# Kernel optimization log

Hardware: AMD Instinct MI355X
Metric: run time of the kernel (lower is better)

The kernel has to match this reference:

```python
import jax, jax.numpy as jnp
import numpy as np

B, S, HID = 1, 2048, 2048
H, KV, D = 16, 8, 128          # heads, kv heads, head_dim
EPS = 1e-6
THETA_T, THETA_HW = 1000000.0, 10000.0
SCALE = D ** -0.5
NEG = -1e9


def _rms(x, w):
    xf = x.astype(jnp.float32)
    var = jnp.mean(xf * xf, axis=-1, keepdims=True)
    return (w * (xf * jax.lax.rsqrt(var + EPS))).astype(x.dtype)


def _rope_cs(pos, theta, half_dim):
    # Module builds RoPE with head_dim = 2*half_dim then takes every-other freq:
    # exponents arange(0, 2*half_dim, 4) / (2*half_dim)  -> half_dim//2 freqs
    dim2 = 2 * half_dim
    inv_freq = 1.0 / theta ** (jnp.arange(0, dim2, 4, dtype=jnp.float32) / dim2)
    freqs = pos.astype(jnp.float32)[:, None] * inv_freq[None, :]   # [S, half_dim//2]
    emb = jnp.concatenate([freqs, freqs], axis=-1)                 # [S, half_dim]
    return jnp.cos(emb), jnp.sin(emb)


def _rot_half(x):
    d = x.shape[-1] // 2
    return jnp.concatenate([-x[..., d:], x[..., :d]], axis=-1)


def _apply_rope(q, k, cos, sin):
    cos = cos[None, None]  # [1,1,S,dim]
    sin = sin[None, None]
    return q * cos + _rot_half(q) * sin, k * cos + _rot_half(k) * sin


def setup_inputs() -> dict:
    key = jax.random.key(0)
    ks = jax.random.split(key, 10)
    hidden_states = jax.random.normal(ks[0], (B, S, HID), jnp.float32)
    indexes = jax.random.randint(ks[1], (3, S), 0, S)
    causal = jnp.tril(jnp.ones((S, S), bool))
    attention_mask = jnp.where(causal, 0.0, NEG).astype(jnp.float32)[None, None]
    qkv_w = jax.random.normal(ks[2], ((H + 2 * KV) * D, HID), jnp.float32) * 0.02
    qkv_b = jax.random.normal(ks[3], ((H + 2 * KV) * D,), jnp.float32) * 0.02
    o_w = jax.random.normal(ks[4], (HID, H * D), jnp.float32) * 0.02
    o_b = jax.random.normal(ks[5], (HID,), jnp.float32) * 0.02
    q_norm_w = jnp.ones((D // 2,), jnp.float32)
    k_norm_w = jnp.ones((D // 2,), jnp.float32)
    q_norm_hw_w = jnp.ones((D // 2,), jnp.float32)
    k_norm_hw_w = jnp.ones((D // 2,), jnp.float32)
    return dict(hidden_states=hidden_states, indexes=indexes, attention_mask=attention_mask,
                qkv_w=qkv_w, qkv_b=qkv_b, o_w=o_w, o_b=o_b,
                q_norm_w=q_norm_w, k_norm_w=k_norm_w,
                q_norm_hw_w=q_norm_hw_w, k_norm_hw_w=k_norm_hw_w)


def reference(hidden_states, indexes, attention_mask, qkv_w, qkv_b, o_w, o_b,
              q_norm_w, k_norm_w, q_norm_hw_w, k_norm_hw_w):
    b, s, _ = hidden_states.shape
    qkv = hidden_states @ qkv_w.T + qkv_b
    q, k, v = jnp.split(qkv, [H * D, H * D + KV * D], axis=-1)
    q = q.reshape(b, s, H, D)
    k = k.reshape(b, s, KV, D)
    v = v.reshape(b, s, KV, D)

    # split head_dim into time half and hw half
    q_t, q_hw = jnp.split(q, 2, axis=-1)
    k_t, k_hw = jnp.split(k, 2, axis=-1)
    q_t = jnp.swapaxes(_rms(q_t, q_norm_w), 1, 2)       # [B,H,S,D/2]
    k_t = jnp.swapaxes(_rms(k_t, k_norm_w), 1, 2)
    q_hw = jnp.swapaxes(_rms(q_hw, q_norm_hw_w), 1, 2)
    k_hw = jnp.swapaxes(_rms(k_hw, k_norm_hw_w), 1, 2)
    q_h, q_ww = jnp.split(q_hw, 2, axis=-1)             # [B,H,S,D/4]
    k_h, k_ww = jnp.split(k_hw, 2, axis=-1)

    cos_t, sin_t = _rope_cs(indexes[0], THETA_T, D // 2)
    q_t, k_t = _apply_rope(q_t, k_t, cos_t, sin_t)
    cos_h, sin_h = _rope_cs(indexes[1], THETA_HW, D // 4)
    q_h, k_h = _apply_rope(q_h, k_h, cos_h, sin_h)
    cos_w, sin_w = _rope_cs(indexes[2], THETA_HW, D // 4)
    q_ww, k_ww = _apply_rope(q_ww, k_ww, cos_w, sin_w)

    query = jnp.concatenate([q_t, q_h, q_ww], axis=-1)  # [B,H,S,D]
    keyst = jnp.concatenate([k_t, k_h, k_ww], axis=-1)  # [B,KV,S,D]
    value = jnp.swapaxes(v, 1, 2)                       # [B,KV,S,D]

    n_rep = H // KV
    keyst = jnp.repeat(keyst, n_rep, axis=1)
    value = jnp.repeat(value, n_rep, axis=1)

    scores = jnp.einsum('bhsd,bhtd->bhst', query, keyst) * SCALE + attention_mask
    probs = jax.nn.softmax(scores.astype(jnp.float32), axis=-1).astype(query.dtype)
    attn = jnp.einsum('bhst,bhtd->bhsd', probs, value)
    attn = jnp.swapaxes(attn, 1, 2).reshape(b, s, H * D)
    return attn @ o_w.T + o_b
```

## Files before the change

### kernel.cpp

```cpp
#include <hip/hip_runtime.h>

typedef __bf16 bf16;
typedef __bf16 bf16x4 __attribute__((ext_vector_type(4)));
typedef __bf16 bf16x8 __attribute__((ext_vector_type(8)));
typedef float f32x4 __attribute__((ext_vector_type(4)));

#define S_LEN 2048
#define HIDDEN 2048
#define NH 16
#define NKV 8
#define HD 128
#define QKV_N 4096

#define PSLOT 66560

__device__ __forceinline__ void async_load16(const void* g, void* l) {
  __builtin_amdgcn_global_load_lds((const __attribute__((address_space(1))) unsigned int*)g,
                                   (__attribute__((address_space(3))) unsigned int*)l,
                                   16, 0, 0);
}

template <int C>
__device__ __forceinline__ float dpp_f(float x) {
  return __builtin_bit_cast(float, __builtin_amdgcn_mov_dpp(
      __builtin_bit_cast(int, x), C, 0xF, 0xF, true));
}
__device__ __forceinline__ float rowmax16(float x) {
  x = fmaxf(x, dpp_f<0x128>(x));
  x = fmaxf(x, dpp_f<0x124>(x));
  x = fmaxf(x, dpp_f<0x122>(x));
  x = fmaxf(x, dpp_f<0x121>(x));
  return x;
}
__device__ __forceinline__ float rowsum16(float x) {
  x += dpp_f<0x128>(x);
  x += dpp_f<0x124>(x);
  x += dpp_f<0x122>(x);
  x += dpp_f<0x121>(x);
  return x;
}

__global__ __launch_bounds__(256)
void cvt_pair(const float* __restrict__ s1, bf16* __restrict__ d1, int n1,
              const float* __restrict__ s2, bf16* __restrict__ d2, int n2) {
  int i = (blockIdx.x * 256 + threadIdx.x) * 4;
  const float* s;
  bf16* d;
  int j;
  if (i < n1) { s = s1; d = d1; j = i; }
  else        { s = s2; d = d2; j = i - n1; if (j >= n2) return; }
  float4 v = *(const float4*)(s + j);
  bf16x4 o = {(bf16)v.x, (bf16)v.y, (bf16)v.z, (bf16)v.w};
  *(bf16x4*)(d + j) = o;
}

template <int WRITE_BF16>
__global__ __launch_bounds__(256)
void gemm_bt(const bf16* __restrict__ A, const bf16* __restrict__ B,
             const float* __restrict__ bias, void* __restrict__ Cout,
             int M, int N, int K) {
  __shared__ bf16 As[2][128 * 64];
  __shared__ bf16 Bs[2][128 * 64];
  const int tid = threadIdx.x;
  const int w = tid >> 6, lane = tid & 63;
  const int quad = lane >> 4, l15 = lane & 15;
  const int wm = w >> 1, wn = w & 1;
  const int m0 = blockIdx.y * 128, n0 = blockIdx.x * 128;

  f32x4 acc[4][4];
#pragma unroll
  for (int i = 0; i < 4; i++)
#pragma unroll
    for (int j = 0; j < 4; j++) acc[i][j] = (f32x4){0.f, 0.f, 0.f, 0.f};

  const int crow = lane >> 2;
  const int ccol = (lane & 3) * 8;

#pragma unroll
  for (int q = 0; q < 4; q++) {
    int c = w * 4 + q, rb = c >> 1, kh = c & 1;
    async_load16(A + (size_t)(m0 + rb * 16 + crow) * K + kh * 32 + ccol,
                 (char*)As[0] + c * 1024);
    async_load16(B + (size_t)(n0 + rb * 16 + crow) * K + kh * 32 + ccol,
                 (char*)Bs[0] + c * 1024);
  }

  int cur = 0;
  for (int k0 = 0; k0 < K; k0 += 64) {
    __asm__ __volatile__("s_waitcnt vmcnt(0)" ::: "memory");
    __syncthreads();
    if (k0 + 64 < K) {
#pragma unroll
      for (int q = 0; q < 4; q++) {
        int c = w * 4 + q, rb = c >> 1, kh = c & 1;
        async_load16(A + (size_t)(m0 + rb * 16 + crow) * K + k0 + 64 + kh * 32 + ccol,
                     (char*)As[cur ^ 1] + c * 1024);
        async_load16(B + (size_t)(n0 + rb * 16 + crow) * K + k0 + 64 + kh * 32 + ccol,
                     (char*)Bs[cur ^ 1] + c * 1024);
      }
    }
    bf16x8 af[4][2], bfr[4][2];
#pragma unroll
    for (int i = 0; i < 4; i++)
#pragma unroll
      for (int kk = 0; kk < 2; kk++)
        af[i][kk] = *(const bf16x8*)((const char*)As[cur] +
                                     ((wm * 4 + i) * 2 + kk) * 1024 + l15 * 64 + quad * 16);
#pragma unroll
    for (int j = 0; j < 4; j++)
#pragma unroll
      for (int kk = 0; kk < 2; kk++)
        bfr[j][kk] = *(const bf16x8*)((const char*)Bs[cur] +
                                      ((wn * 4 + j) * 2 + kk) * 1024 + l15 * 64 + quad * 16);
#pragma unroll
    for (int kk = 0; kk < 2; kk++)
#pragma unroll
      for (int i = 0; i < 4; i++)
#pragma unroll
        for (int j = 0; j < 4; j++)
          acc[i][j] = __builtin_amdgcn_mfma_f32_16x16x32_bf16(af[i][kk], bfr[j][kk],
                                                              acc[i][j], 0, 0, 0);
    cur ^= 1;
  }

#pragma unroll
  for (int i = 0; i < 4; i++) {
#pragma unroll
    for (int j = 0; j < 4; j++) {
      int col = n0 + wn * 64 + j * 16 + l15;
      float bv = bias[col];
#pragma unroll
      for (int r = 0; r < 4; r++) {
        int row = m0 + wm * 64 + i * 16 + quad * 4 + r;
        float v = acc[i][j][r] + bv;
        if (WRITE_BF16)
          ((bf16*)Cout)[(size_t)row * N + col] = (bf16)v;
        else
          ((float*)Cout)[(size_t)row * N + col] = v;
      }
    }
  }
}

__global__ __launch_bounds__(256)
void gemm_qkv(const bf16* __restrict__ A, const bf16* __restrict__ B,
              const float* __restrict__ bias, const int* __restrict__ idx,
              const float* __restrict__ qnw, const float* __restrict__ knw,
              const float* __restrict__ qnhw, const float* __restrict__ knhw,
              bf16* __restrict__ Qb, bf16* __restrict__ Kb, bf16* __restrict__ VT) {
  const int K = HIDDEN;
  __shared__ __align__(16) char smem[128 * 132 * 4];
  char* Abase = smem;
  char* Bbase = smem + 32768;
  const int tid = threadIdx.x;
  const int w = tid >> 6, lane = tid & 63;
  const int quad = lane >> 4, l15 = lane & 15;
  const int wm = w >> 1, wn = w & 1;
  const int m0 = blockIdx.y * 128, n0 = blockIdx.x * 128;

  f32x4 acc[4][4];
#pragma unroll
  for (int i = 0; i < 4; i++)
#pragma unroll
    for (int j = 0; j < 4; j++) acc[i][j] = (f32x4){0.f, 0.f, 0.f, 0.f};

  const int crow = lane >> 2;
  const int ccol = (lane & 3) * 8;

#pragma unroll
  for (int q = 0; q < 4; q++) {
    int c = w * 4 + q, rb = c >> 1, kh = c & 1;
    async_load16(A + (size_t)(m0 + rb * 16 + crow) * K + kh * 32 + ccol,
                 Abase + c * 1024);
    async_load16(B + (size_t)(n0 + rb * 16 + crow) * K + kh * 32 + ccol,
                 Bbase + c * 1024);
  }

  int cur = 0;
  for (int k0 = 0; k0 < K; k0 += 64) {
    __asm__ __volatile__("s_waitcnt vmcnt(0)" ::: "memory");
    __syncthreads();
    if (k0 + 64 < K) {
#pragma unroll
      for (int q = 0; q < 4; q++) {
        int c = w * 4 + q, rb = c >> 1, kh = c & 1;
        async_load16(A + (size_t)(m0 + rb * 16 + crow) * K + k0 + 64 + kh * 32 + ccol,
                     Abase + (cur ^ 1) * 16384 + c * 1024);
        async_load16(B + (size_t)(n0 + rb * 16 + crow) * K + k0 + 64 + kh * 32 + ccol,
                     Bbase + (cur ^ 1) * 16384 + c * 1024);
      }
    }
    bf16x8 af[4][2], bfr[4][2];
#pragma unroll
    for (int i = 0; i < 4; i++)
#pragma unroll
      for (int kk = 0; kk < 2; kk++)
        af[i][kk] = *(const bf16x8*)(Abase + cur * 16384 +
                                     ((wm * 4 + i) * 2 + kk) * 1024 + l15 * 64 + quad * 16);
#pragma unroll
    for (int j = 0; j < 4; j++)
#pragma unroll
      for (int kk = 0; kk < 2; kk++)
        bfr[j][kk] = *(const bf16x8*)(Bbase + cur * 16384 +
                                      ((wn * 4 + j) * 2 + kk) * 1024 + l15 * 64 + quad * 16);
#pragma unroll
    for (int kk = 0; kk < 2; kk++)
#pragma unroll
      for (int i = 0; i < 4; i++)
#pragma unroll
        for (int j = 0; j < 4; j++)
          acc[i][j] = __builtin_amdgcn_mfma_f32_16x16x32_bf16(af[i][kk], bfr[j][kk],
                                                              acc[i][j], 0, 0, 0);
    cur ^= 1;
  }

  const int nb = blockIdx.x;

  if (nb >= 24) {
    const int kv = nb - 24;
#pragma unroll
    for (int i = 0; i < 4; i++) {
#pragma unroll
      for (int j = 0; j < 4; j++) {
        const int d = wn * 64 + j * 16 + l15;
        const float bv = bias[n0 + d];
        bf16x4 o;
#pragma unroll
        for (int r = 0; r < 4; r++) o[r] = (bf16)(acc[i][j][r] + bv);
        *(bf16x4*)(VT + ((size_t)(kv * HD + d)) * S_LEN +
                   (m0 + wm * 64 + i * 16 + quad * 4)) = o;
      }
    }
    return;
  }

  __syncthreads();
  float* tile = (float*)smem;
#pragma unroll
  for (int i = 0; i < 4; i++) {
#pragma unroll
    for (int j = 0; j < 4; j++) {
      const int col = wn * 64 + j * 16 + l15;
      const float bv = bias[n0 + col];
      const int row = wm * 64 + i * 16 + quad * 4;
#pragma unroll
      for (int r = 0; r < 4; r++)
        tile[(row + r) * 132 + col] = acc[i][j][r] + bv;
    }
  }
  __syncthreads();

  const bool isq = (nb < 16);
  const int head = isq ? nb : nb - 16;
  const int row = tid & 127;
  const int half = tid >> 7;
  const int srow = m0 + row;
  const float* trow = tile + row * 132 + half * 64;

  float ss = 0.f;
#pragma unroll
  for (int g = 0; g < 16; g++) {
    f32x4 v = *(const f32x4*)(trow + g * 4);
    ss += v[0] * v[0] + v[1] * v[1] + v[2] * v[2] + v[3] * v[3];
  }
  const float inv = rsqrtf(ss * (1.f / 64.f) + 1e-6f);
  const float oscale = isq ? 0.12751745f : 1.0f;
  const float* wt = (half == 0) ? (isq ? qnw : knw) : (isq ? qnhw : knhw);
  bf16* op = (isq ? Qb : Kb) + (size_t)head * S_LEN * HD + (size_t)srow * HD + half * 64;

  if (half == 0) {
    const float pos = (float)idx[srow];
#pragma unroll
    for (int g = 0; g < 8; g++) {
      f32x4 a = *(const f32x4*)(trow + g * 4);
      f32x4 b = *(const f32x4*)(trow + (g + 8) * 4);
      bf16x4 oa, ob;
#pragma unroll
      for (int e = 0; e < 4; e++) {
        const int d = g * 4 + e;
        float ya = a[e] * inv * wt[d];
        float yb = b[e] * inv * wt[32 + d];
        float s_, c_;
        sincosf(pos * exp2f(-(float)d * 0.6228615177913804f), &s_, &c_);
        oa[e] = (bf16)((ya * c_ - yb * s_) * oscale);
        ob[e] = (bf16)((yb * c_ + ya * s_) * oscale);
      }
      *(bf16x4*)(op + g * 4) = oa;
      *(bf16x4*)(op + 32 + g * 4) = ob;
    }
  } else {
    const float p1 = (float)idx[S_LEN + srow];
    const float p2 = (float)idx[2 * S_LEN + srow];
#pragma unroll
    for (int gg = 0; gg < 8; gg++) {
      const int g = (gg < 4) ? gg : (gg + 4);
      const float pos = (gg < 4) ? p1 : p2;
      f32x4 a = *(const f32x4*)(trow + g * 4);
      f32x4 b = *(const f32x4*)(trow + (g + 4) * 4);
      bf16x4 oa, ob;
#pragma unroll
      for (int e = 0; e < 4; e++) {
        const int jj = g * 4 + e;
        const int fi = (g & 3) * 4 + e;
        float ya = a[e] * inv * wt[jj];
        float yb = b[e] * inv * wt[jj + 16];
        float s_, c_;
        sincosf(pos * exp2f(-(float)fi * 0.8304820237218406f), &s_, &c_);
        oa[e] = (bf16)((ya * c_ - yb * s_) * oscale);
        ob[e] = (bf16)((yb * c_ + ya * s_) * oscale);
      }
      *(bf16x4*)(op + g * 4) = oa;
      *(bf16x4*)(op + (g + 4) * 4) = ob;
    }
  }
}

__global__ __launch_bounds__(256)
void attn_fused(const bf16* __restrict__ Qb, const bf16* __restrict__ Kb,
                const bf16* __restrict__ VT, bf16* __restrict__ attnO,
                char* __restrict__ Opart) {
  __shared__ bf16 Kbuf[2][8192];
  __shared__ bf16 Vbuf[8192];
  __shared__ __align__(16) bf16 Ps[4][2][16][72];
  const int tid = threadIdx.x;
  const int w = tid >> 6, lane = tid & 63;
  const int quad = lane >> 4, l15 = lane & 15;
  const int b = blockIdx.x;
  const int h = b & 15;
  const int cid = b >> 4;
  int G, c, nc;
  if (cid < 5)       { G = cid;          c = 0;     nc = 1; }
  else if (cid < 17) { int t = cid - 5;  G = 5 + (t >> 1);  c = t & 1; nc = 2; }
  else               { int t = cid - 17; G = 11 + t / 3;    c = t % 3; nc = 3; }
  const int nT = 2 * G + 2;
  const int tBeg = c * 11;
  const int tEnd = (tBeg + 11 < nT) ? (tBeg + 11) : nT;
  const int tCap0 = 2 * G + 1;
  const int kv = h >> 1;
  const int qr0h[2] = {G * 128 + w * 16, G * 128 + 64 + w * 16};

  const bf16* Qg = Qb + (size_t)h * S_LEN * HD;
  const bf16* Kg = Kb + (size_t)kv * S_LEN * HD;
  const bf16* Vg = VT + (size_t)kv * HD * S_LEN;

  const bf16* ksrc = Kg + (size_t)(w * 16 + l15) * HD + quad * 8;
  const bf16* vsrc = Vg + (size_t)(2 * w * 16 + l15) * S_LEN + quad * 8;

  bf16x8 aq[2][4];
#pragma unroll
  for (int bb = 0; bb < 2; bb++)
#pragma unroll
    for (int kc = 0; kc < 4; kc++)
      aq[bb][kc] = *(const bf16x8*)(Qg + (size_t)(qr0h[bb] + l15) * HD + kc * 32 + quad * 8);

  float m2[2][4], li[2][4];
  f32x4 Oacc[2][8];
#pragma unroll
  for (int bb = 0; bb < 2; bb++) {
#pragma unroll
    for (int r = 0; r < 4; r++) { m2[bb][r] = -1e30f; li[bb][r] = 0.f; }
#pragma unroll
    for (int dt = 0; dt < 8; dt++) Oacc[bb][dt] = (f32x4){0.f, 0.f, 0.f, 0.f};
  }

#pragma unroll
  for (int kc = 0; kc < 4; kc++)
    async_load16(ksrc + (size_t)(tBeg << 6) * HD + kc * 32,
                 (char*)Kbuf[tBeg & 1] + (w * 4 + kc) * 1024);

  for (int tt = tBeg; tt < tEnd; ++tt) {
    const int t0 = tt << 6;
    const int cur = tt & 1;
    const bool more = (tt + 1 < tEnd);
    const bool do0 = (tt < tCap0);
    __asm__ __volatile__("s_waitcnt vmcnt(0)" ::: "memory");
    __syncthreads();

#pragma unroll
    for (int e = 0; e < 2; e++)
#pragma unroll
      for (int half = 0; half < 2; half++)
        async_load16(vsrc + (size_t)e * 16 * S_LEN + t0 + half * 32,
                     (char*)Vbuf + (half * 8 + 2 * w + e) * 1024);
    if (more) {
#pragma unroll
      for (int kc = 0; kc < 4; kc++)
        async_load16(ksrc + (size_t)(t0 + 64) * HD + kc * 32,
                     (char*)Kbuf[cur ^ 1] + (w * 4 + kc) * 1024);
    }

#pragma unroll
    for (int bb = 0; bb < 2; bb++) {
      if (bb == 0 && !do0) continue;
      const int qr0 = qr0h[bb];
      f32x4 sacc[4];
#pragma unroll
      for (int nt = 0; nt < 4; nt++) {
        sacc[nt] = (f32x4){0.f, 0.f, 0.f, 0.f};
#pragma unroll
        for (int kc = 0; kc < 4; kc++) {
          bf16x8 bk = *(const bf16x8*)((const char*)Kbuf[cur] + (nt * 4 + kc) * 1024 + lane * 16);
          sacc[nt] = __builtin_amdgcn_mfma_f32_16x16x32_bf16(aq[bb][kc], bk, sacc[nt], 0, 0, 0);
        }
      }
      const bool full = (t0 + 64 <= qr0);
      float mxv[4];
      bool need = false;
#pragma unroll
      for (int r = 0; r < 4; r++) {
        if (!full) {
          const int mrow = qr0 + quad * 4 + r;
          const int cb = t0 + l15;
          if (cb > mrow) sacc[0][r] = -1e30f;
          if (cb + 16 > mrow) sacc[1][r] = -1e30f;
          if (cb + 32 > mrow) sacc[2][r] = -1e30f;
          if (cb + 48 > mrow) sacc[3][r] = -1e30f;
        }
        mxv[r] = rowmax16(fmaxf(fmaxf(sacc[0][r], sacc[1][r]), fmaxf(sacc[2][r], sacc[3][r])));
        need = need || (mxv[r] > m2[bb][r] + 8.f);
      }
      if (__any(need ? 1 : 0)) {
#pragma unroll
        for (int r = 0; r < 4; r++) {
          float mnew = fmaxf(m2[bb][r], mxv[r]);
          float a = exp2f(m2[bb][r] - mnew);
          li[bb][r] *= a;
#pragma unroll
          for (int dt = 0; dt < 8; dt++) Oacc[bb][dt][r] *= a;
          m2[bb][r] = mnew;
        }
      }
#pragma unroll
      for (int r = 0; r < 4; r++) {
        float p0 = exp2f(sacc[0][r] - m2[bb][r]);
        float p1 = exp2f(sacc[1][r] - m2[bb][r]);
        float p2 = exp2f(sacc[2][r] - m2[bb][r]);
        float p3 = exp2f(sacc[3][r] - m2[bb][r]);
        li[bb][r] += rowsum16((p0 + p1) + (p2 + p3));
        Ps[w][bb][quad * 4 + r][l15] = (bf16)p0;
        Ps[w][bb][quad * 4 + r][16 + l15] = (bf16)p1;
        Ps[w][bb][quad * 4 + r][32 + l15] = (bf16)p2;
        Ps[w][bb][quad * 4 + r][48 + l15] = (bf16)p3;
      }
    }
    __asm__ __volatile__("s_waitcnt lgkmcnt(0)" ::: "memory");
    if (more)
      __asm__ __volatile__("s_waitcnt vmcnt(4)" ::: "memory");
    else
      __asm__ __volatile__("s_waitcnt vmcnt(0)" ::: "memory");

#pragma unroll
    for (int bb = 0; bb < 2; bb++) {
      if (bb == 0 && !do0) continue;
#pragma unroll
      for (int half = 0; half < 2; half++) {
        bf16x8 ap = *(const bf16x8*)(&Ps[w][bb][l15][half * 32 + quad * 8]);
#pragma unroll
        for (int dt = 0; dt < 8; dt++) {
          bf16x8 bv = *(const bf16x8*)((const char*)Vbuf + (half * 8 + dt) * 1024 + lane * 16);
          Oacc[bb][dt] = __builtin_amdgcn_mfma_f32_16x16x32_bf16(ap, bv, Oacc[bb][dt], 0, 0, 0);
        }
      }
    }
  }

  if (nc > 1) {
    char* slot = Opart + (size_t)((cid - 5) * 16 + h) * PSLOT;
    float* Op = (float*)slot;
    float* mlp = (float*)(slot + 65536);
#pragma unroll
    for (int bb = 0; bb < 2; bb++) {
#pragma unroll
      for (int r = 0; r < 4; r++) {
        const int row = bb * 64 + w * 16 + quad * 4 + r;
#pragma unroll
        for (int dt = 0; dt < 8; dt++)
          Op[row * 128 + dt * 16 + l15] = Oacc[bb][dt][r];
        if (l15 == 0) {
          mlp[row * 2 + 0] = m2[bb][r];
          mlp[row * 2 + 1] = li[bb][r];
        }
      }
    }
  } else {
#pragma unroll
    for (int bb = 0; bb < 2; bb++) {
#pragma unroll
      for (int r = 0; r < 4; r++) {
        float invl = 1.f / li[bb][r];
        int srow = qr0h[bb] + quad * 4 + r;
#pragma unroll
        for (int dt = 0; dt < 8; dt++)
          attnO[(size_t)srow * HIDDEN + h * HD + dt * 16 + l15] = (bf16)(Oacc[bb][dt][r] * invl);
      }
    }
  }
}

__global__ __launch_bounds__(256)
void merge_cvt(const char* __restrict__ Opart, bf16* __restrict__ attnO,
               const float* __restrict__ ow, bf16* __restrict__ owB) {
  const int t = threadIdx.x;
  {
    int i = (blockIdx.x * 256 + t) * 4;
    float4 v = *(const float4*)(ow + i);
    bf16x4 o = {(bf16)v.x, (bf16)v.y, (bf16)v.z, (bf16)v.w};
    *(bf16x4*)(owB + i) = o;
  }
  if (blockIdx.x >= 176) return;

  const int h = blockIdx.x & 15;
  const int bandIdx = blockIdx.x >> 4;
  const int G = 5 + bandIdx;
  const int nc = (G <= 10) ? 2 : 3;
  const int cid0 = (G <= 10) ? (5 + (G - 5) * 2) : (17 + (G - 11) * 3);
  const char* s0 = Opart + (size_t)((cid0 - 5) * 16 + h) * PSLOT;
  const char* s1 = s0 + (size_t)16 * PSLOT;
  const char* s2 = s0 + (size_t)32 * PSLOT;
  const float* O0 = (const float*)s0;
  const float* O1 = (const float*)s1;
  const float* O2 = (const float*)s2;
  const float* ML0 = (const float*)(s0 + 65536);
  const float* ML1 = (const float*)(s1 + 65536);
  const float* ML2 = (const float*)(s2 + 65536);
#pragma unroll
  for (int it = 0; it < 16; ++it) {
    int e = it * 256 + t;
    int row = e >> 5, d = (e & 31) * 4;
    float m0 = ML0[row * 2], l0 = ML0[row * 2 + 1];
    float m1 = ML1[row * 2], l1 = ML1[row * 2 + 1];
    float m2v = -1e30f, l2v = 0.f;
    if (nc == 3) { m2v = ML2[row * 2]; l2v = ML2[row * 2 + 1]; }
    float m = fmaxf(fmaxf(m0, m1), m2v);
    float a0 = exp2f(m0 - m), a1 = exp2f(m1 - m), a2 = exp2f(m2v - m);
    float inv = 1.f / (a0 * l0 + a1 * l1 + a2 * l2v);
    f32x4 x0 = *(const f32x4*)(O0 + row * 128 + d);
    f32x4 x1 = *(const f32x4*)(O1 + row * 128 + d);
    f32x4 x2 = (f32x4){0.f, 0.f, 0.f, 0.f};
    if (nc == 3) x2 = *(const f32x4*)(O2 + row * 128 + d);
    int srow = G * 128 + row;
    bf16x4 o;
#pragma unroll
    for (int j = 0; j < 4; j++)
      o[j] = (bf16)((a0 * x0[j] + a1 * x1[j] + a2 * x2[j]) * inv);
    *(bf16x4*)(attnO + (size_t)srow * HIDDEN + h * HD + d) = o;
  }
}

extern "C" void kernel_launch(void* const* d_in, const int* in_sizes, int n_in,
                              void* d_out, int out_size, void* d_ws, size_t ws_size,
                              hipStream_t stream) {
  const float* hidden = (const float*)d_in[0];
  const int* idx = (const int*)d_in[1];
  const float* qkv_w = (const float*)d_in[3];
  const float* qkv_b = (const float*)d_in[4];
  const float* o_w = (const float*)d_in[5];
  const float* o_b = (const float*)d_in[6];
  const float* qnw = (const float*)d_in[7];
  const float* knw = (const float*)d_in[8];
  const float* qnhw = (const float*)d_in[9];
  const float* knhw = (const float*)d_in[10];

  char* ws = (char*)d_ws;
  bf16* hB    = (bf16*)(ws);
  bf16* qwB   = (bf16*)(ws + (8u << 20));
  bf16* Qb    = (bf16*)(ws + (40u << 20));
  bf16* Kb    = (bf16*)(ws + (48u << 20));
  bf16* VT    = (bf16*)(ws + (52u << 20));
  char* Opart = ws;
  bf16* owB   = (bf16*)(ws + (40u << 20));
  bf16* attn  = (bf16*)(ws + (32u << 20));

  cvt_pair<<<12288, 256, 0, stream>>>(hidden, hB, HIDDEN * S_LEN,
                                      qkv_w, qwB, QKV_N * HIDDEN);

  gemm_qkv<<<dim3(QKV_N / 128, S_LEN / 128), 256, 0, stream>>>(
      hB, qwB, qkv_b, idx, qnw, knw, qnhw, knhw, Qb, Kb, VT);

  attn_fused<<<512, 256, 0, stream>>>(Qb, Kb, VT, attn, Opart);

  merge_cvt<<<4096, 256, 0, stream>>>(Opart, attn, o_w, owB);

  gemm_bt<0><<<dim3(HIDDEN / 128, S_LEN / 128), 256, 0, stream>>>(
      attn, owB, o_b, (float*)d_out, S_LEN, HIDDEN, HIDDEN);
}
```

Before: 267.5 us.

## Shrink attention query tile to 64 rows and drop K double-buffering

Each attention block now handles 64 query rows instead of 128, and the chunk/split schedule and merge kernel are rebuilt for 1008 blocks in 32 bands. The K tile is no longer double-buffered: K and V load synchronously at each iteration with a full wait. The aim is more blocks for better load balance and occupancy, plus less LDS and register use. The cost is that each K/V tile is reused by half as many queries, so K/V global traffic roughly doubles, and the load latency is no longer overlapped with compute.

Result: slower. 280.6 us (+4.9%).

```diff
diff --git a/kernel.cpp b/kernel.cpp
--- a/kernel.cpp
+++ b/kernel.cpp
@@ -12,7 +12,7 @@
 #define HD 128
 #define QKV_N 4096
 
-#define PSLOT 66560
+#define PSLOT 33280
 
 __device__ __forceinline__ void async_load16(const void* g, void* l) {
   __builtin_amdgcn_global_load_lds((const __attribute__((address_space(1))) unsigned int*)g,
@@ -319,25 +319,24 @@
 void attn_fused(const bf16* __restrict__ Qb, const bf16* __restrict__ Kb,
                 const bf16* __restrict__ VT, bf16* __restrict__ attnO,
                 char* __restrict__ Opart) {
-  __shared__ bf16 Kbuf[2][8192];
+  __shared__ bf16 Kbuf[8192];
   __shared__ bf16 Vbuf[8192];
-  __shared__ __align__(16) bf16 Ps[4][2][16][72];
+  __shared__ __align__(16) bf16 Ps[4][16][72];
   const int tid = threadIdx.x;
   const int w = tid >> 6, lane = tid & 63;
   const int quad = lane >> 4, l15 = lane & 15;
   const int b = blockIdx.x;
   const int h = b & 15;
   const int cid = b >> 4;
-  int G, c, nc;
-  if (cid < 5)       { G = cid;          c = 0;     nc = 1; }
-  else if (cid < 17) { int t = cid - 5;  G = 5 + (t >> 1);  c = t & 1; nc = 2; }
-  else               { int t = cid - 17; G = 11 + t / 3;    c = t % 3; nc = 3; }
-  const int nT = 2 * G + 2;
+  int g, c, nc;
+  if (cid < 11)      { g = cid;          c = 0;            nc = 1; }
+  else if (cid < 33) { int t = cid - 11; g = 11 + (t >> 1); c = t & 1; nc = 2; }
+  else               { int t = cid - 33; g = 22 + t / 3;    c = t % 3; nc = 3; }
+  const int nT = g + 1;
   const int tBeg = c * 11;
   const int tEnd = (tBeg + 11 < nT) ? (tBeg + 11) : nT;
-  const int tCap0 = 2 * G + 1;
+  const int qr0 = g * 64 + w * 16;
   const int kv = h >> 1;
-  const int qr0h[2] = {G * 128 + w * 16, G * 128 + 64 + w * 16};
 
   const bf16* Qg = Qb + (size_t)h * S_LEN * HD;
   const bf16* Kg = Kb + (size_t)kv * S_LEN * HD;
@@ -346,153 +345,119 @@
   const bf16* ksrc = Kg + (size_t)(w * 16 + l15) * HD + quad * 8;
   const bf16* vsrc = Vg + (size_t)(2 * w * 16 + l15) * S_LEN + quad * 8;
 
-  bf16x8 aq[2][4];
-#pragma unroll
-  for (int bb = 0; bb < 2; bb++)
-#pragma unroll
-    for (int kc = 0; kc < 4; kc++)
-      aq[bb][kc] = *(const bf16x8*)(Qg + (size_t)(qr0h[bb] + l15) * HD + kc * 32 + quad * 8);
-
-  float m2[2][4], li[2][4];
-  f32x4 Oacc[2][8];
-#pragma unroll
-  for (int bb = 0; bb < 2; bb++) {
-#pragma unroll
-    for (int r = 0; r < 4; r++) { m2[bb][r] = -1e30f; li[bb][r] = 0.f; }
-#pragma unroll
-    for (int dt = 0; dt < 8; dt++) Oacc[bb][dt] = (f32x4){0.f, 0.f, 0.f, 0.f};
-  }
-
+  bf16x8 aq[4];
 #pragma unroll
   for (int kc = 0; kc < 4; kc++)
-    async_load16(ksrc + (size_t)(tBeg << 6) * HD + kc * 32,
-                 (char*)Kbuf[tBeg & 1] + (w * 4 + kc) * 1024);
+    aq[kc] = *(const bf16x8*)(Qg + (size_t)(qr0 + l15) * HD + kc * 32 + quad * 8);
+
+  float m2[4], li[4];
+  f32x4 Oacc[8];
+#pragma unroll
+  for (int r = 0; r < 4; r++) { m2[r] = -1e30f; li[r] = 0.f; }
+#pragma unroll
+  for (int dt = 0; dt < 8; dt++) Oacc[dt] = (f32x4){0.f, 0.f, 0.f, 0.f};
 
   for (int tt = tBeg; tt < tEnd; ++tt) {
     const int t0 = tt << 6;
-    const int cur = tt & 1;
-    const bool more = (tt + 1 < tEnd);
-    const bool do0 = (tt < tCap0);
-    __asm__ __volatile__("s_waitcnt vmcnt(0)" ::: "memory");
     __syncthreads();
-
+#pragma unroll
+    for (int kc = 0; kc < 4; kc++)
+      async_load16(ksrc + (size_t)t0 * HD + kc * 32, (char*)Kbuf + (w * 4 + kc) * 1024);
 #pragma unroll
     for (int e = 0; e < 2; e++)
 #pragma unroll
       for (int half = 0; half < 2; half++)
         async_load16(vsrc + (size_t)e * 16 * S_LEN + t0 + half * 32,
                      (char*)Vbuf + (half * 8 + 2 * w + e) * 1024);
-    if (more) {
-#pragma unroll
-      for (int kc = 0; kc < 4; kc++)
-        async_load16(ksrc + (size_t)(t0 + 64) * HD + kc * 32,
-                     (char*)Kbuf[cur ^ 1] + (w * 4 + kc) * 1024);
-    }
-
-#pragma unroll
-    for (int bb = 0; bb < 2; bb++) {
-      if (bb == 0 && !do0) continue;
-      const int qr0 = qr0h[bb];
-      f32x4 sacc[4];
-#pragma unroll
-      for (int nt = 0; nt < 4; nt++) {
-        sacc[nt] = (f32x4){0.f, 0.f, 0.f, 0.f};
-#pragma unroll
-        for (int kc = 0; kc < 4; kc++) {
-          bf16x8 bk = *(const bf16x8*)((const char*)Kbuf[cur] + (nt * 4 + kc) * 1024 + lane * 16);
-          sacc[nt] = __builtin_amdgcn_mfma_f32_16x16x32_bf16(aq[bb][kc], bk, sacc[nt], 0, 0, 0);
-        }
-      }
-      const bool full = (t0 + 64 <= qr0);
-      float mxv[4];
-      bool need = false;
+    __asm__ __volatile__("s_waitcnt vmcnt(0)" ::: "memory");
+    __syncthreads();
+
+    f32x4 sacc[4];
+#pragma unroll
+    for (int nt = 0; nt < 4; nt++) {
+      sacc[nt] = (f32x4){0.f, 0.f, 0.f, 0.f};
+#pragma unroll
+      for (int kc = 0; kc < 4; kc++) {
+        bf16x8 bk = *(const bf16x8*)((const char*)Kbuf + (nt * 4 + kc) * 1024 + lane * 16);
+        sacc[nt] = __builtin_amdgcn_mfma_f32_16x16x32_bf16(aq[kc], bk, sacc[nt], 0, 0, 0);
+      }
+    }
+
+    const bool full = (t0 + 64 <= qr0);
+    float mxv[4];
+    bool need = false;
+#pragma unroll
+    for (int r = 0; r < 4; r++) {
+      if (!full) {
+        const int mrow = qr0 + quad * 4 + r;
+        const int cb = t0 + l15;
+        if (cb > mrow) sacc[0][r] = -1e30f;
+        if (cb + 16 > mrow) sacc[1][r] = -1e30f;
+        if (cb + 32 > mrow) sacc[2][r] = -1e30f;
+        if (cb + 48 > mrow) sacc[3][r] = -1e30f;
+      }
+      mxv[r] = rowmax16(fmaxf(fmaxf(sacc[0][r], sacc[1][r]), fmaxf(sacc[2][r], sacc[3][r])));
+      need = need || (mxv[r] > m2[r] + 8.f);
+    }
+    if (__any(need ? 1 : 0)) {
 #pragma unroll
       for (int r = 0; r < 4; r++) {
-        if (!full) {
-          const int mrow = qr0 + quad * 4 + r;
-          const int cb = t0 + l15;
-          if (cb > mrow) sacc[0][r] = -1e30f;
-          if (cb + 16 > mrow) sacc[1][r] = -1e30f;
-          if (cb + 32 > mrow) sacc[2][r] = -1e30f;
-          if (cb + 48 > mrow) sacc[3][r] = -1e30f;
-        }
-        mxv[r] = rowmax16(fmaxf(fmaxf(sacc[0][r], sacc[1][r]), fmaxf(sacc[2][r], sacc[3][r])));
-        need = need || (mxv[r] > m2[bb][r] + 8.f);
-      }
-      if (__any(need ? 1 : 0)) {
-#pragma unroll
-        for (int r = 0; r < 4; r++) {
-          float mnew = fmaxf(m2[bb][r], mxv[r]);
-          float a = exp2f(m2[bb][r] - mnew);
-          li[bb][r] *= a;
-#pragma unroll
-          for (int dt = 0; dt < 8; dt++) Oacc[bb][dt][r] *= a;
-          m2[bb][r] = mnew;
-        }
-      }
-#pragma unroll
-      for (int r = 0; r < 4; r++) {
-        float p0 = exp2f(sacc[0][r] - m2[bb][r]);
-        float p1 = exp2f(sacc[1][r] - m2[bb][r]);
-        float p2 = exp2f(sacc[2][r] - m2[bb][r]);
-        float p3 = exp2f(sacc[3][r] - m2[bb][r]);
-        li[bb][r] += rowsum16((p0 + p1) + (p2 + p3));
-        Ps[w][bb][quad * 4 + r][l15] = (bf16)p0;
-        Ps[w][bb][quad * 4 + r][16 + l15] = (bf16)p1;
-        Ps[w][bb][quad * 4 + r][32 + l15] = (bf16)p2;
-        Ps[w][bb][quad * 4 + r][48 + l15] = (bf16)p3;
-      }
+        float mnew = fmaxf(m2[r], mxv[r]);
+        float a = exp2f(m2[r] - mnew);
+        li[r] *= a;
+#pragma unroll
+        for (int dt = 0; dt < 8; dt++) Oacc[dt][r] *= a;
+        m2[r] = mnew;
+      }
+    }
+#pragma unroll
+    for (int r = 0; r < 4; r++) {
+      float p0 = exp2f(sacc[0][r] - m2[r]);
+      float p1 = exp2f(sacc[1][r] - m2[r]);
+      float p2 = exp2f(sacc[2][r] - m2[r]);
+      float p3 = exp2f(sacc[3][r] - m2[r]);
+      li[r] += rowsum16((p0 + p1) + (p2 + p3));
+      Ps[w][quad * 4 + r][l15] = (bf16)p0;
+      Ps[w][quad * 4 + r][16 + l15] = (bf16)p1;
+      Ps[w][quad * 4 + r][32 + l15] = (bf16)p2;
+      Ps[w][quad * 4 + r][48 + l15] = (bf16)p3;
     }
     __asm__ __volatile__("s_waitcnt lgkmcnt(0)" ::: "memory");
-    if (more)
-      __asm__ __volatile__("s_waitcnt vmcnt(4)" ::: "memory");
-    else
-      __asm__ __volatile__("s_waitcnt vmcnt(0)" ::: "memory");
-
-#pragma unroll
-    for (int bb = 0; bb < 2; bb++) {
-      if (bb == 0 && !do0) continue;
-#pragma unroll
-      for (int half = 0; half < 2; half++) {
-        bf16x8 ap = *(const bf16x8*)(&Ps[w][bb][l15][half * 32 + quad * 8]);
-#pragma unroll
-        for (int dt = 0; dt < 8; dt++) {
-          bf16x8 bv = *(const bf16x8*)((const char*)Vbuf + (half * 8 + dt) * 1024 + lane * 16);
-          Oacc[bb][dt] = __builtin_amdgcn_mfma_f32_16x16x32_bf16(ap, bv, Oacc[bb][dt], 0, 0, 0);
-        }
+
+#pragma unroll
+    for (int half = 0; half < 2; half++) {
+      bf16x8 ap = *(const bf16x8*)(&Ps[w][l15][half * 32 + quad * 8]);
+#pragma unroll
+      for (int dt = 0; dt < 8; dt++) {
+        bf16x8 bv = *(const bf16x8*)((const char*)Vbuf + (half * 8 + dt) * 1024 + lane * 16);
+        Oacc[dt] = __builtin_amdgcn_mfma_f32_16x16x32_bf16(ap, bv, Oacc[dt], 0, 0, 0);
       }
     }
   }
 
   if (nc > 1) {
-    char* slot = Opart + (size_t)((cid - 5) * 16 + h) * PSLOT;
+    char* slot = Opart + (size_t)((cid - 11) * 16 + h) * PSLOT;
     float* Op = (float*)slot;
-    float* mlp = (float*)(slot + 65536);
-#pragma unroll
-    for (int bb = 0; bb < 2; bb++) {
-#pragma unroll
-      for (int r = 0; r < 4; r++) {
-        const int row = bb * 64 + w * 16 + quad * 4 + r;
-#pragma unroll
-        for (int dt = 0; dt < 8; dt++)
-          Op[row * 128 + dt * 16 + l15] = Oacc[bb][dt][r];
-        if (l15 == 0) {
-          mlp[row * 2 + 0] = m2[bb][r];
-          mlp[row * 2 + 1] = li[bb][r];
-        }
+    float* mlp = (float*)(slot + 32768);
+#pragma unroll
+    for (int r = 0; r < 4; r++) {
+      const int row = w * 16 + quad * 4 + r;
+#pragma unroll
+      for (int dt = 0; dt < 8; dt++)
+        Op[row * 128 + dt * 16 + l15] = Oacc[dt][r];
+      if (l15 == 0) {
+        mlp[row * 2 + 0] = m2[r];
+        mlp[row * 2 + 1] = li[r];
       }
     }
   } else {
 #pragma unroll
-    for (int bb = 0; bb < 2; bb++) {
-#pragma unroll
-      for (int r = 0; r < 4; r++) {
-        float invl = 1.f / li[bb][r];
-        int srow = qr0h[bb] + quad * 4 + r;
-#pragma unroll
-        for (int dt = 0; dt < 8; dt++)
-          attnO[(size_t)srow * HIDDEN + h * HD + dt * 16 + l15] = (bf16)(Oacc[bb][dt][r] * invl);
-      }
+    for (int r = 0; r < 4; r++) {
+      float invl = 1.f / li[r];
+      int srow = qr0 + quad * 4 + r;
+#pragma unroll
+      for (int dt = 0; dt < 8; dt++)
+        attnO[(size_t)srow * HIDDEN + h * HD + dt * 16 + l15] = (bf16)(Oacc[dt][r] * invl);
     }
   }
 }
@@ -507,24 +472,24 @@
     bf16x4 o = {(bf16)v.x, (bf16)v.y, (bf16)v.z, (bf16)v.w};
     *(bf16x4*)(owB + i) = o;
   }
-  if (blockIdx.x >= 176) return;
+  if (blockIdx.x >= 336) return;
 
   const int h = blockIdx.x & 15;
   const int bandIdx = blockIdx.x >> 4;
-  const int G = 5 + bandIdx;
-  const int nc = (G <= 10) ? 2 : 3;
-  const int cid0 = (G <= 10) ? (5 + (G - 5) * 2) : (17 + (G - 11) * 3);
-  const char* s0 = Opart + (size_t)((cid0 - 5) * 16 + h) * PSLOT;
+  const int g = 11 + bandIdx;
+  const int nc = (g <= 21) ? 2 : 3;
+  const int cid0 = (g <= 21) ? (11 + (g - 11) * 2) : (33 + (g - 22) * 3);
+  const char* s0 = Opart + (size_t)((cid0 - 11) * 16 + h) * PSLOT;
   const char* s1 = s0 + (size_t)16 * PSLOT;
   const char* s2 = s0 + (size_t)32 * PSLOT;
   const float* O0 = (const float*)s0;
   const float* O1 = (const float*)s1;
   const float* O2 = (const float*)s2;
-  const float* ML0 = (const float*)(s0 + 65536);
-  const float* ML1 = (const float*)(s1 + 65536);
-  const float* ML2 = (const float*)(s2 + 65536);
-#pragma unroll
-  for (int it = 0; it < 16; ++it) {
+  const float* ML0 = (const float*)(s0 + 32768);
+  const float* ML1 = (const float*)(s1 + 32768);
+  const float* ML2 = (const float*)(s2 + 32768);
+#pragma unroll
+  for (int it = 0; it < 8; ++it) {
     int e = it * 256 + t;
     int row = e >> 5, d = (e & 31) * 4;
     float m0 = ML0[row * 2], l0 = ML0[row * 2 + 1];
@@ -538,7 +503,7 @@
     f32x4 x1 = *(const f32x4*)(O1 + row * 128 + d);
     f32x4 x2 = (f32x4){0.f, 0.f, 0.f, 0.f};
     if (nc == 3) x2 = *(const f32x4*)(O2 + row * 128 + d);
-    int srow = G * 128 + row;
+    int srow = g * 64 + row;
     bf16x4 o;
 #pragma unroll
     for (int j = 0; j < 4; j++)
@@ -577,7 +542,7 @@
   gemm_qkv<<<dim3(QKV_N / 128, S_LEN / 128), 256, 0, stream>>>(
       hB, qwB, qkv_b, idx, qnw, knw, qnhw, knhw, Qb, Kb, VT);
 
-  attn_fused<<<512, 256, 0, stream>>>(Qb, Kb, VT, attn, Opart);
+  attn_fused<<<1008, 256, 0, stream>>>(Qb, Kb, VT, attn, Opart);
 
   merge_cvt<<<4096, 256, 0, stream>>>(Opart, attn, o_w, owB);
 
```
